# Kernel tuning notes

Hardware: AMD Instinct MI355X
Metric: run time of the kernel (lower is better)

Reference implementation:

```python
import jax, jax.numpy as jnp
import numpy as np

B = 64          # graphs per batch
N = 1500        # nodes per graph (equal sizes -> vectorized sortpool)
NT = B * N      # total nodes
DEG = 16        # avg in-degree
E_PER = N * DEG # edges per graph
F_IN = 128
K = 30          # sortpool k
LATENT = [32, 32, 32, 1]  # total 97
TOTAL_LAT = sum(LATENT)
OUT_DIM = 128


def setup_inputs() -> dict:
    key = jax.random.key(0)
    ks = jax.random.split(key, 16)
    node_feat = jax.random.normal(ks[0], (NT, F_IN), dtype=jnp.float32)
    # edges constrained within each graph (block-diagonal adjacency)
    offs = (jnp.arange(B, dtype=jnp.int32) * N)[:, None]
    edge_src = (jax.random.randint(ks[1], (B, E_PER), 0, N, dtype=jnp.int32) + offs).reshape(-1)
    edge_dst = (jax.random.randint(ks[2], (B, E_PER), 0, N, dtype=jnp.int32) + offs).reshape(-1)

    def lin(k, fan_in, shape):
        return jax.random.normal(k, shape, dtype=jnp.float32) * (1.0 / np.sqrt(fan_in))

    inp = dict(node_feat=node_feat, edge_src=edge_src, edge_dst=edge_dst)
    dims = [F_IN] + LATENT
    for i in range(4):
        inp[f'W{i+1}'] = lin(ks[3 + i], dims[i], (dims[i], dims[i + 1]))
        inp[f'b{i+1}'] = jnp.zeros((dims[i + 1],), jnp.float32)
    inp['conv1_w'] = lin(ks[8], TOTAL_LAT, (16, TOTAL_LAT))   # Conv1d(1,16,97,stride=97)
    inp['conv1_b'] = jnp.zeros((16,), jnp.float32)
    inp['conv2_w'] = lin(ks[9], 16 * 5, (32, 16, 5))          # Conv1d(16,32,5)
    inp['conv2_b'] = jnp.zeros((32,), jnp.float32)
    inp['out_w'] = lin(ks[10], 352, (352, OUT_DIM))
    inp['out_b'] = jnp.zeros((OUT_DIM,), jnp.float32)
    return inp


def reference(node_feat, edge_src, edge_dst, W1, b1, W2, b2, W3, b3, W4, b4,
              conv1_w, conv1_b, conv2_w, conv2_b, out_w, out_b):
    # node degrees (+1 for self loop), from in-edges
    deg = jax.ops.segment_sum(jnp.ones_like(edge_dst, jnp.float32), edge_dst, num_segments=NT)
    node_degs = (deg + 1.0)[:, None]

    # 4 graph-conv layers: (A @ h + h) -> Linear -> /deg -> tanh, concat features
    h = node_feat
    layers = []
    for W, b in ((W1, b1), (W2, b2), (W3, b3), (W4, b4)):
        agg = jax.ops.segment_sum(h[edge_src], edge_dst, num_segments=NT) + h
        h = jnp.tanh((agg @ W + b) / node_degs)
        layers.append(h)
    feat = jnp.concatenate(layers, axis=1)  # [NT, 97]

    # sortpooling: top-k nodes per graph by the last channel
    sort_ch = feat[:, -1].reshape(B, N)
    _, idx = jax.lax.top_k(sort_ch, K)                    # [B, K]
    gidx = (idx + (jnp.arange(B, dtype=idx.dtype) * N)[:, None]).reshape(-1)
    pooled = feat[gidx].reshape(B, K, TOTAL_LAT)          # [B, K, 97]

    # Conv1d(1,16,97,stride=97) over flattened [B,1,K*97] == per-slot linear
    c1 = jax.nn.relu(jnp.einsum('bkd,od->bok', pooled, conv1_w) + conv1_b[None, :, None])  # [B,16,K]
    mp = c1.reshape(B, 16, K // 2, 2).max(axis=-1)        # MaxPool1d(2,2) -> [B,16,15]
    c2 = jax.lax.conv_general_dilated(mp, conv2_w, (1,), 'VALID',
                                      dimension_numbers=('NCH', 'OIH', 'NCH'))
    c2 = jax.nn.relu(c2 + conv2_b[None, :, None])         # [B,32,11]
    dense = c2.reshape(B, -1)                             # [B,352]
    return jax.nn.relu(dense @ out_w + out_b)             # relu(relu(x)) == relu(x)
```

## Files before the change

kernel.cpp:

```cpp
#include <hip/hip_runtime.h>

constexpr int B = 64, N = 1500, NT = B * N;
constexpr int E_PER = 24000, E_TOT = B * E_PER;
constexpr int NQ = 4, NPQ = N / NQ;
constexpr int CAP = 9216;
constexpr int F_INN = 128, K = 30, TOT = 97;
constexpr int NB_G = 47;
constexpr int GEMM_TILES = NT / 128;

__global__ __launch_bounds__(256) void prep(const int* __restrict__ src, const int* __restrict__ dst,
                                            ushort* __restrict__ csr, int* __restrict__ rowst,
                                            int* __restrict__ degi, float* __restrict__ degf,
                                            float* __restrict__ tA,
                                            const float* __restrict__ nf, const float* __restrict__ W1) {
    __shared__ union {
        struct { int hist[NPQ]; uint4 slice[CAP / 8]; int wtot; } c;
        struct { float hs[32][128]; float Ws[32][32]; } g;
    } u;
    int bid = blockIdx.x, t = threadIdx.x;

    if (bid < B * NQ) {
        ushort* csr_l = (ushort*)u.c.slice;
        int g = bid >> 2, q = bid & 3;
        int gbase = g * N, qlo = q * NPQ;
        const int4* d4 = reinterpret_cast<const int4*>(dst + (size_t)g * E_PER);
        const int4* s4 = reinterpret_cast<const int4*>(src + (size_t)g * E_PER);

        for (int i = t; i < NPQ; i += 256) u.c.hist[i] = 0;
        __syncthreads();
        for (int i = t; i < E_PER / 4; i += 256) {
            int4 d = d4[i];
            int x0 = d.x - gbase - qlo, x1 = d.y - gbase - qlo;
            int x2 = d.z - gbase - qlo, x3 = d.w - gbase - qlo;
            if ((unsigned)x0 < (unsigned)NPQ) atomicAdd(&u.c.hist[x0], 1);
            if ((unsigned)x1 < (unsigned)NPQ) atomicAdd(&u.c.hist[x1], 1);
            if ((unsigned)x2 < (unsigned)NPQ) atomicAdd(&u.c.hist[x2], 1);
            if ((unsigned)x3 < (unsigned)NPQ) atomicAdd(&u.c.hist[x3], 1);
        }
        __syncthreads();

        int local[3];
        int sum = 0, x = 0;
        if (t < 128) {
#pragma unroll
            for (int i = 0; i < 3; ++i) {
                int v = t * 3 + i;
                int d = (v < NPQ) ? u.c.hist[v] : 0;
                local[i] = d;
                sum += (d + 7) & ~7;
            }
            x = sum;
            int lane = t & 63;
#pragma unroll
            for (int m = 1; m < 64; m <<= 1) {
                int y = __shfl_up(x, m, 64);
                if (lane >= m) x += y;
            }
        }
        if (t == 63) u.c.wtot = x;
        __syncthreads();
        if (t < 128) {
            int base = (t >= 64) ? u.c.wtot : 0;
            int run = base + x - sum;
            int rbase = (g * NQ + q) * CAP;
#pragma unroll
            for (int i = 0; i < 3; ++i) {
                int v = t * 3 + i;
                if (v < NPQ) {
                    int gv = gbase + qlo + v;
                    rowst[gv] = rbase + run;
                    degi[gv] = local[i];
                    degf[gv] = (float)(local[i] + 1);
                    u.c.hist[v] = run;
                    run += (local[i] + 7) & ~7;
                }
            }
        }
        __syncthreads();
        for (int i = t; i < E_PER / 4; i += 256) {
            int4 d = d4[i];
            int4 s = s4[i];
            int x0 = d.x - gbase - qlo, x1 = d.y - gbase - qlo;
            int x2 = d.z - gbase - qlo, x3 = d.w - gbase - qlo;
            if ((unsigned)x0 < (unsigned)NPQ) { int p = atomicAdd(&u.c.hist[x0], 1); csr_l[p] = (ushort)(s.x - gbase); }
            if ((unsigned)x1 < (unsigned)NPQ) { int p = atomicAdd(&u.c.hist[x1], 1); csr_l[p] = (ushort)(s.y - gbase); }
            if ((unsigned)x2 < (unsigned)NPQ) { int p = atomicAdd(&u.c.hist[x2], 1); csr_l[p] = (ushort)(s.z - gbase); }
            if ((unsigned)x3 < (unsigned)NPQ) { int p = atomicAdd(&u.c.hist[x3], 1); csr_l[p] = (ushort)(s.w - gbase); }
        }
        __syncthreads();
        for (int v = t; v < NPQ; v += 256)
            for (int sft = u.c.hist[v]; sft & 7; ++sft) csr_l[sft] = (ushort)(qlo + v);
        __syncthreads();
        uint4* cg = reinterpret_cast<uint4*>(csr + (size_t)(g * NQ + q) * CAP);
        for (int i = t; i < CAP / 8; i += 256)
            cg[i] = u.c.slice[i];
    } else {
        int tile = bid - B * NQ;
        int wv = t >> 6, lane = t & 63;
        int v0 = tile * 128;
        int og = wv * 8;
        float acc[2][8];
#pragma unroll
        for (int i = 0; i < 2; ++i)
#pragma unroll
            for (int j = 0; j < 8; ++j) acc[i][j] = 0.f;

        for (int kc = 0; kc < F_INN; kc += 32) {
            __syncthreads();
            {
                int n = t >> 1, kh = (t & 1) * 16;
                const float* hp = nf + (size_t)(v0 + n) * F_INN + kc + kh;
                const float4* hp4 = reinterpret_cast<const float4*>(hp);
                float4 a = hp4[0], b = hp4[1], c = hp4[2], d = hp4[3];
                u.g.hs[kh + 0][n] = a.x;  u.g.hs[kh + 1][n] = a.y;  u.g.hs[kh + 2][n] = a.z;  u.g.hs[kh + 3][n] = a.w;
                u.g.hs[kh + 4][n] = b.x;  u.g.hs[kh + 5][n] = b.y;  u.g.hs[kh + 6][n] = b.z;  u.g.hs[kh + 7][n] = b.w;
                u.g.hs[kh + 8][n] = c.x;  u.g.hs[kh + 9][n] = c.y;  u.g.hs[kh + 10][n] = c.z; u.g.hs[kh + 11][n] = c.w;
                u.g.hs[kh + 12][n] = d.x; u.g.hs[kh + 13][n] = d.y; u.g.hs[kh + 14][n] = d.z; u.g.hs[kh + 15][n] = d.w;
                int r = t >> 3, c4 = (t & 7) * 4;
                float4 w = *reinterpret_cast<const float4*>(W1 + (size_t)(kc + r) * 32 + c4);
                *reinterpret_cast<float4*>(&u.g.Ws[r][c4]) = w;
            }
            __syncthreads();
#pragma unroll
            for (int k = 0; k < 32; ++k) {
                float2 hv = *reinterpret_cast<const float2*>(&u.g.hs[k][2 * lane]);
                float4 w0 = *reinterpret_cast<const float4*>(&u.g.Ws[k][og]);
                float4 w1 = *reinterpret_cast<const float4*>(&u.g.Ws[k][og + 4]);
                acc[0][0] += hv.x * w0.x; acc[0][1] += hv.x * w0.y; acc[0][2] += hv.x * w0.z; acc[0][3] += hv.x * w0.w;
                acc[0][4] += hv.x * w1.x; acc[0][5] += hv.x * w1.y; acc[0][6] += hv.x * w1.z; acc[0][7] += hv.x * w1.w;
                acc[1][0] += hv.y * w0.x; acc[1][1] += hv.y * w0.y; acc[1][2] += hv.y * w0.z; acc[1][3] += hv.y * w0.w;
                acc[1][4] += hv.y * w1.x; acc[1][5] += hv.y * w1.y; acc[1][6] += hv.y * w1.z; acc[1][7] += hv.y * w1.w;
            }
        }
#pragma unroll
        for (int i = 0; i < 2; ++i) {
            float* op = tA + (size_t)(v0 + 2 * lane + i) * 32 + og;
            float4 r0 = {acc[i][0], acc[i][1], acc[i][2], acc[i][3]};
            float4 r1 = {acc[i][4], acc[i][5], acc[i][6], acc[i][7]};
            reinterpret_cast<float4*>(op)[0] = r0;
            reinterpret_cast<float4*>(op)[1] = r1;
        }
    }
}

template <int FUSE>
__global__ __launch_bounds__(256) void agg_f(const float* __restrict__ t,
                                             const ushort* __restrict__ csr, const int* __restrict__ rowst,
                                             const int* __restrict__ degi, const float* __restrict__ degf,
                                             const float* __restrict__ bias, const float* __restrict__ Wn,
                                             float* __restrict__ hout, float* __restrict__ tn) {
    __shared__ float Ws[1024];
    __shared__ float outs[32][32];
    if (FUSE == 32) {
        for (int i = threadIdx.x; i < 1024; i += 256) Ws[i] = Wn[i];
    }
    int bid = blockIdx.x;
    int xcd = bid & 7, j = bid >> 3;
    int g = xcd + 8 * (j / NB_G);
    int nb = j % NB_G;
    int nl = threadIdx.x >> 3;
    int f4 = threadIdx.x & 7;
    int vl = nb * 32 + nl;
    bool valid = vl < N;
    int v = g * N + vl;
    int gb8 = g * N * 8;
    const float4* t4v = reinterpret_cast<const float4*>(t);
    float4 out = {0.f, 0.f, 0.f, 0.f};
    if (valid) {
        float4 tself = t4v[(unsigned)(v * 8 + f4)];
        int e0 = rowst[v];
        int dc = degi[v];
        int pc = (dc + 7) & ~7;
        float scale = (float)(1 + dc - pc);
        float4 acc = {scale * tself.x, scale * tself.y, scale * tself.z, scale * tself.w};
        float4 s1 = {0.f, 0.f, 0.f, 0.f}, s2 = {0.f, 0.f, 0.f, 0.f};
        float4 s3 = {0.f, 0.f, 0.f, 0.f}, s4v = {0.f, 0.f, 0.f, 0.f};
        for (int e = 0; e < pc; e += 8) {
            ushort4 ia = *reinterpret_cast<const ushort4*>(csr + e0 + e);
            ushort4 ib = *reinterpret_cast<const ushort4*>(csr + e0 + e + 4);
            float4 x0 = t4v[(unsigned)(gb8 + ia.x * 8 + f4)];
            float4 x1 = t4v[(unsigned)(gb8 + ia.y * 8 + f4)];
            float4 x2 = t4v[(unsigned)(gb8 + ia.z * 8 + f4)];
            float4 x3 = t4v[(unsigned)(gb8 + ia.w * 8 + f4)];
            float4 x4 = t4v[(unsigned)(gb8 + ib.x * 8 + f4)];
            float4 x5 = t4v[(unsigned)(gb8 + ib.y * 8 + f4)];
            float4 x6 = t4v[(unsigned)(gb8 + ib.z * 8 + f4)];
            float4 x7 = t4v[(unsigned)(gb8 + ib.w * 8 + f4)];
            s1.x += x0.x + x1.x; s1.y += x0.y + x1.y; s1.z += x0.z + x1.z; s1.w += x0.w + x1.w;
            s2.x += x2.x + x3.x; s2.y += x2.y + x3.y; s2.z += x2.z + x3.z; s2.w += x2.w + x3.w;
            s3.x += x4.x + x5.x; s3.y += x4.y + x5.y; s3.z += x4.z + x5.z; s3.w += x4.w + x5.w;
            s4v.x += x6.x + x7.x; s4v.y += x6.y + x7.y; s4v.z += x6.z + x7.z; s4v.w += x6.w + x7.w;
        }
        acc.x += (s1.x + s2.x) + (s3.x + s4v.x);
        acc.y += (s1.y + s2.y) + (s3.y + s4v.y);
        acc.z += (s1.z + s2.z) + (s3.z + s4v.z);
        acc.w += (s1.w + s2.w) + (s3.w + s4v.w);
        float4 bv = *reinterpret_cast<const float4*>(bias + f4 * 4);
        float inv = 1.0f / degf[v];
        out.x = tanhf((acc.x + bv.x) * inv);
        out.y = tanhf((acc.y + bv.y) * inv);
        out.z = tanhf((acc.z + bv.z) * inv);
        out.w = tanhf((acc.w + bv.w) * inv);
        reinterpret_cast<float4*>(hout)[(unsigned)(v * 8 + f4)] = out;
    }
    if (FUSE == 32) {
        *reinterpret_cast<float4*>(&outs[nl][f4 * 4]) = out;
        __syncthreads();
        if (valid) {
            float4 s = {0.f, 0.f, 0.f, 0.f};
#pragma unroll
            for (int ff = 0; ff < 32; ++ff) {
                float h = outs[nl][ff];
                float4 wr = *reinterpret_cast<const float4*>(&Ws[ff * 32 + f4 * 4]);
                s.x += h * wr.x; s.y += h * wr.y; s.z += h * wr.z; s.w += h * wr.w;
            }
            reinterpret_cast<float4*>(tn)[(unsigned)(v * 8 + f4)] = s;
        }
    } else if (valid) {
        float4 w4 = *reinterpret_cast<const float4*>(Wn + f4 * 4);
        float p = out.x * w4.x + out.y * w4.y + out.z * w4.z + out.w * w4.w;
        p += __shfl_xor(p, 4, 64);
        p += __shfl_xor(p, 2, 64);
        p += __shfl_xor(p, 1, 64);
        if (f4 == 0) tn[v] = p;
    }
}

__global__ __launch_bounds__(512) void sort_head(const float* __restrict__ hc1, const float* __restrict__ hc2,
                                                 const float* __restrict__ hc3, const float* __restrict__ t4,
                                                 const ushort* __restrict__ csr, const int* __restrict__ rowst,
                                                 const int* __restrict__ degi, const float* __restrict__ degf,
                                                 const float* __restrict__ b4,
                                                 const float* __restrict__ c1w, const float* __restrict__ c1b,
                                                 const float* __restrict__ c2w, const float* __restrict__ c2b,
                                                 const float* __restrict__ ow, const float* __restrict__ ob,
                                                 float* __restrict__ out) {
    __shared__ float ts[N];
    __shared__ unsigned int svals[N];
    __shared__ float fvals[N];
    __shared__ int hist[2048];
    __shared__ int canA[N], canB[N];
    __shared__ int winners[32];
    __shared__ int wsum[8];
    __shared__ int st_need, st_ncand, st_tb, st_cab, st_nwin;
    __shared__ int topk_s[K];
    __shared__ float pooled[K][TOT];
    __shared__ float c1[16][K];
    __shared__ float mp[16][16];
    __shared__ float dense[352];
    __shared__ float part[4][128];

    int g = blockIdx.x, t = threadIdx.x;
    int gbase = g * N;
    int lane = t & 63, w = t >> 6;

    for (int v = t; v < N; v += 512) ts[v] = t4[gbase + v];
    if (t == 0) { st_need = K; st_nwin = 0; }
    __syncthreads();
    {
        float b4v = b4[0];
        for (int v = t; v < N; v += 512) {
            int gv = gbase + v;
            int e0 = rowst[gv], dc = degi[gv];
            int pc = (dc + 7) & ~7;
            float scale = (float)(1 + dc - pc);
            float a0 = 0.f, a1 = 0.f, a2 = 0.f, a3 = 0.f;
            for (int e = 0; e < pc; e += 4) {
                ushort4 s4 = *reinterpret_cast<const ushort4*>(csr + e0 + e);
                a0 += ts[s4.x];
                a1 += ts[s4.y];
                a2 += ts[s4.z];
                a3 += ts[s4.w];
            }
            float h = tanhf((scale * ts[v] + (a0 + a1) + (a2 + a3) + b4v) / degf[gv]);
            fvals[v] = h;
            unsigned int b = __float_as_uint(h);
            svals[v] = (b & 0x80000000u) ? ~b : (b | 0x80000000u);
        }
    }
    __syncthreads();

    auto mkkey = [&](int idx) {
        return ((unsigned long long)svals[idx] << 31) | (unsigned int)(0x7FFFFFFF - idx);
    };

    const int SHIFTS[6] = {52, 41, 30, 19, 8, 0};
    int curN = N;
    int src = 0;
    for (int pass = 0; pass < 6; ++pass) {
        int shift = SHIFTS[pass];
        int mask = (pass == 5) ? 0xFF : 0x7FF;
        for (int i = t; i < 2048; i += 512) hist[i] = 0;
        if (t == 0) st_ncand = 0;
        __syncthreads();
        for (int i = t; i < curN; i += 512) {
            int idx = (src == 0) ? i : (src == 1 ? canA[i] : canB[i]);
            int d = (int)((mkkey(idx) >> shift) & mask);
            atomicAdd(&hist[d], 1);
        }
        __syncthreads();
        int need = st_need;
        int c[4];
        int s = 0;
#pragma unroll
        for (int u = 0; u < 4; ++u) { c[u] = hist[2047 - (4 * t + u)]; s += c[u]; }
        int x = s;
#pragma unroll
        for (int m = 1; m < 64; m <<= 1) {
            int y = __shfl_up(x, m, 64);
            if (lane >= m) x += y;
        }
        if (lane == 63) wsum[w] = x;
        __syncthreads();
        int woff = 0;
        for (int ww = 0; ww < w; ++ww) woff += wsum[ww];
        int A = woff + x - s;
#pragma unroll
        for (int u = 0; u < 4; ++u) {
            if (A < need && need <= A + c[u]) { st_tb = 2047 - (4 * t + u); st_cab = A; }
            A += c[u];
        }
        __syncthreads();
        int tb = st_tb, cab = st_cab;
        int* dst = (src == 1) ? canB : canA;
        for (int i = t; i < curN; i += 512) {
            int idx = (src == 0) ? i : (src == 1 ? canA[i] : canB[i]);
            int d = (int)((mkkey(idx) >> shift) & mask);
            if (d > tb) {
                int p = atomicAdd(&st_nwin, 1);
                winners[p] = idx;
            } else if (d == tb) {
                int p = atomicAdd(&st_ncand, 1);
                dst[p] = idx;
            }
        }
        __syncthreads();
        int ncand = st_ncand;
        need -= cab;
        if (t == 0) st_need = need;
        if (ncand == need) {
            int base = st_nwin;
            for (int i = t; i < ncand; i += 512) winners[base + i] = dst[i];
            __syncthreads();
            break;
        }
        curN = ncand;
        src = (src == 1) ? 2 : 1;
        __syncthreads();
    }

    if (t < 64) {
        unsigned long long key = (t < K) ? mkkey(winners[t]) : 0ull;
        unsigned long long kk = ~key;
#pragma unroll
        for (int k = 2; k <= 64; k <<= 1) {
#pragma unroll
            for (int j = k >> 1; j > 0; j >>= 1) {
                unsigned long long o = __shfl_xor(kk, j, 64);
                bool keepMin = ((t & j) == 0) == ((t & k) == 0);
                kk = keepMin ? (kk < o ? kk : o) : (kk > o ? kk : o);
            }
        }
        key = ~kk;
        if (t < K) topk_s[t] = 0x7FFFFFFF - (int)(unsigned int)(key & 0x7FFFFFFFu);
    }
    __syncthreads();

    for (int i = t; i < K * TOT; i += 512) {
        int k = i / TOT, d = i % TOT;
        int vloc = topk_s[k];
        int gi = gbase + vloc;
        float val = (d < 32) ? hc1[(size_t)gi * 32 + d]
                  : (d < 64) ? hc2[(size_t)gi * 32 + d - 32]
                  : (d < 96) ? hc3[(size_t)gi * 32 + d - 64]
                             : fvals[vloc];
        pooled[k][d] = val;
    }
    __syncthreads();
    for (int i = t; i < 16 * K; i += 512) {
        int o = i / K, k = i % K;
        float s = c1b[o];
        for (int d = 0; d < TOT; ++d) s += pooled[k][d] * c1w[o * TOT + d];
        c1[o][k] = fmaxf(s, 0.f);
    }
    __syncthreads();
    for (int i = t; i < 16 * 15; i += 512) {
        int o = i / 15, p = i % 15;
        mp[o][p] = fmaxf(c1[o][2 * p], c1[o][2 * p + 1]);
    }
    __syncthreads();
    for (int i = t; i < 352; i += 512) {
        int o = i / 11, p = i % 11;
        float s = c2b[o];
#pragma unroll
        for (int ci = 0; ci < 16; ++ci)
#pragma unroll
            for (int tt = 0; tt < 5; ++tt)
                s += mp[ci][p + tt] * c2w[(o * 16 + ci) * 5 + tt];
        dense[i] = fmaxf(s, 0.f);
    }
    __syncthreads();
    {
        int o = t & 127, q = t >> 7;
        float s = 0.f;
        for (int m = q * 88; m < (q + 1) * 88; ++m) s += dense[m] * ow[m * 128 + o];
        part[q][o] = s;
    }
    __syncthreads();
    if (t < 128) {
        float s = (part[0][t] + part[1][t]) + (part[2][t] + part[3][t]) + ob[t];
        out[g * 128 + t] = fmaxf(s, 0.f);
    }
}

extern "C" void kernel_launch(void* const* d_in, const int* in_sizes, int n_in,
                              void* d_out, int out_size, void* d_ws, size_t ws_size,
                              hipStream_t stream) {
    const float* node_feat = (const float*)d_in[0];
    const int* esrc = (const int*)d_in[1];
    const int* edst = (const int*)d_in[2];
    const float* W1 = (const float*)d_in[3];
    const float* b1 = (const float*)d_in[4];
    const float* W2 = (const float*)d_in[5];
    const float* b2 = (const float*)d_in[6];
    const float* W3 = (const float*)d_in[7];
    const float* b3 = (const float*)d_in[8];
    const float* W4 = (const float*)d_in[9];
    const float* b4 = (const float*)d_in[10];
    const float* c1w = (const float*)d_in[11];
    const float* c1b = (const float*)d_in[12];
    const float* c2w = (const float*)d_in[13];
    const float* c2b = (const float*)d_in[14];
    const float* ow = (const float*)d_in[15];
    const float* ob = (const float*)d_in[16];

    char* ws = (char*)d_ws;
    size_t off = 0;
    auto alloc = [&](size_t bytes) {
        size_t r = off;
        off += (bytes + 255) & ~(size_t)255;
        return r;
    };
    int* deg_i = (int*)(ws + alloc((size_t)NT * 4));
    int* rowst = (int*)(ws + alloc((size_t)NT * 4));
    float* degf = (float*)(ws + alloc((size_t)NT * 4));
    ushort* csr = (ushort*)(ws + alloc((size_t)B * NQ * CAP * 2));
    float* tA = (float*)(ws + alloc((size_t)NT * 32 * 4));
    float* tB = (float*)(ws + alloc((size_t)NT * 32 * 4));
    float* hc1 = (float*)(ws + alloc((size_t)NT * 32 * 4));
    float* hc2 = (float*)(ws + alloc((size_t)NT * 32 * 4));
    float* hc3 = (float*)(ws + alloc((size_t)NT * 32 * 4));
    float* t4 = (float*)(ws + alloc((size_t)NT * 4));

    prep<<<B * NQ + GEMM_TILES, 256, 0, stream>>>(esrc, edst, csr, rowst, deg_i, degf,
                                                  tA, node_feat, W1);

    agg_f<32><<<8 * NB_G * 8, 256, 0, stream>>>(tA, csr, rowst, deg_i, degf, b1, W2, hc1, tB);
    agg_f<32><<<8 * NB_G * 8, 256, 0, stream>>>(tB, csr, rowst, deg_i, degf, b2, W3, hc2, tA);
    agg_f<1><<<8 * NB_G * 8, 256, 0, stream>>>(tA, csr, rowst, deg_i, degf, b3, W4, hc3, t4);

    sort_head<<<B, 512, 0, stream>>>(hc1, hc2, hc3, t4, csr, rowst, deg_i, degf, b4,
                                     c1w, c1b, c2w, c2b, ow, ob, (float*)d_out);
}
```

Baseline: 116.7 us.

## Sort nodes by degree per quarter-graph to balance aggregation wavefront work

The prep kernel now counting-sorts each quarter-graph's nodes by in-degree and writes a permutation array. The aggregation kernels read node indices through this permutation, with 12 blocks per quarter and NB_G raised to 48, so nodes of similar degree share a wavefront. The aim is to cut divergence from the variable-length edge loops. In exchange it adds an indirect load per node and scatters the output writes, which are no longer contiguous.

```diff
diff --git a/kernel.cpp b/kernel.cpp
--- a/kernel.cpp
+++ b/kernel.cpp
@@ -4,17 +4,19 @@
 constexpr int E_PER = 24000, E_TOT = B * E_PER;
 constexpr int NQ = 4, NPQ = N / NQ;
 constexpr int CAP = 9216;
+constexpr int PERM_STRIDE = 384;
 constexpr int F_INN = 128, K = 30, TOT = 97;
-constexpr int NB_G = 47;
+constexpr int NB_G = 48;
 constexpr int GEMM_TILES = NT / 128;
 
 __global__ __launch_bounds__(256) void prep(const int* __restrict__ src, const int* __restrict__ dst,
                                             ushort* __restrict__ csr, int* __restrict__ rowst,
                                             int* __restrict__ degi, float* __restrict__ degf,
+                                            ushort* __restrict__ perm,
                                             float* __restrict__ tA,
                                             const float* __restrict__ nf, const float* __restrict__ W1) {
     __shared__ union {
-        struct { int hist[NPQ]; uint4 slice[CAP / 8]; int wtot; } c;
+        struct { int hist[NPQ]; uint4 slice[CAP / 8]; int wtot; int dh[64]; } c;
         struct { float hs[32][128]; float Ws[32][32]; } g;
     } u;
     int bid = blockIdx.x, t = threadIdx.x;
@@ -27,6 +29,7 @@
         const int4* s4 = reinterpret_cast<const int4*>(src + (size_t)g * E_PER);
 
         for (int i = t; i < NPQ; i += 256) u.c.hist[i] = 0;
+        if (t < 64) u.c.dh[t] = 0;
         __syncthreads();
         for (int i = t; i < E_PER / 4; i += 256) {
             int4 d = d4[i];
@@ -48,6 +51,7 @@
                 int d = (v < NPQ) ? u.c.hist[v] : 0;
                 local[i] = d;
                 sum += (d + 7) & ~7;
+                if (v < NPQ) atomicAdd(&u.c.dh[min(d, 63)], 1);
             }
             x = sum;
             int lane = t & 63;
@@ -59,6 +63,9 @@
         }
         if (t == 63) u.c.wtot = x;
         __syncthreads();
+        int myDeg[3];
+#pragma unroll
+        for (int i = 0; i < 3; ++i) myDeg[i] = (t < 128) ? local[i] : 0;
         if (t < 128) {
             int base = (t >= 64) ? u.c.wtot : 0;
             int run = base + x - sum;
@@ -77,6 +84,28 @@
             }
         }
         __syncthreads();
+        if (t < 64) {
+            int c = u.c.dh[t];
+            int xx = c;
+#pragma unroll
+            for (int m = 1; m < 64; m <<= 1) {
+                int y = __shfl_up(xx, m, 64);
+                if (t >= m) xx += y;
+            }
+            u.c.dh[t] = xx - c;
+        }
+        __syncthreads();
+        if (t < 128) {
+            ushort* pg = perm + (size_t)(g * NQ + q) * PERM_STRIDE;
+#pragma unroll
+            for (int i = 0; i < 3; ++i) {
+                int v = t * 3 + i;
+                if (v < NPQ) {
+                    int pos = atomicAdd(&u.c.dh[min(myDeg[i], 63)], 1);
+                    pg[pos] = (ushort)v;
+                }
+            }
+        }
         for (int i = t; i < E_PER / 4; i += 256) {
             int4 d = d4[i];
             int4 s = s4[i];
@@ -147,6 +176,7 @@
 __global__ __launch_bounds__(256) void agg_f(const float* __restrict__ t,
                                              const ushort* __restrict__ csr, const int* __restrict__ rowst,
                                              const int* __restrict__ degi, const float* __restrict__ degf,
+                                             const ushort* __restrict__ perm,
                                              const float* __restrict__ bias, const float* __restrict__ Wn,
                                              float* __restrict__ hout, float* __restrict__ tn) {
     __shared__ float Ws[1024];
@@ -158,10 +188,13 @@
     int xcd = bid & 7, j = bid >> 3;
     int g = xcd + 8 * (j / NB_G);
     int nb = j % NB_G;
+    int q = nb / 12, slot = nb % 12;
     int nl = threadIdx.x >> 3;
     int f4 = threadIdx.x & 7;
-    int vl = nb * 32 + nl;
-    bool valid = vl < N;
+    int idx = slot * 32 + nl;
+    bool valid = idx < NPQ;
+    int vl = 0;
+    if (valid) vl = q * NPQ + perm[(size_t)(g * NQ + q) * PERM_STRIDE + idx];
     int v = g * N + vl;
     int gb8 = g * N * 8;
     const float4* t4v = reinterpret_cast<const float4*>(t);
@@ -445,6 +478,7 @@
     int* rowst = (int*)(ws + alloc((size_t)NT * 4));
     float* degf = (float*)(ws + alloc((size_t)NT * 4));
     ushort* csr = (ushort*)(ws + alloc((size_t)B * NQ * CAP * 2));
+    ushort* perm = (ushort*)(ws + alloc((size_t)B * NQ * PERM_STRIDE * 2));
     float* tA = (float*)(ws + alloc((size_t)NT * 32 * 4));
     float* tB = (float*)(ws + alloc((size_t)NT * 32 * 4));
     float* hc1 = (float*)(ws + alloc((size_t)NT * 32 * 4));
@@ -453,11 +487,11 @@
     float* t4 = (float*)(ws + alloc((size_t)NT * 4));
 
     prep<<<B * NQ + GEMM_TILES, 256, 0, stream>>>(esrc, edst, csr, rowst, deg_i, degf,
-                                                  tA, node_feat, W1);
-
-    agg_f<32><<<8 * NB_G * 8, 256, 0, stream>>>(tA, csr, rowst, deg_i, degf, b1, W2, hc1, tB);
-    agg_f<32><<<8 * NB_G * 8, 256, 0, stream>>>(tB, csr, rowst, deg_i, degf, b2, W3, hc2, tA);
-    agg_f<1><<<8 * NB_G * 8, 256, 0, stream>>>(tA, csr, rowst, deg_i, degf, b3, W4, hc3, t4);
+                                                  perm, tA, node_feat, W1);
+
+    agg_f<32><<<8 * NB_G * 8, 256, 0, stream>>>(tA, csr, rowst, deg_i, degf, perm, b1, W2, hc1, tB);
+    agg_f<32><<<8 * NB_G * 8, 256, 0, stream>>>(tB, csr, rowst, deg_i, degf, perm, b2, W3, hc2, tA);
+    agg_f<1><<<8 * NB_G * 8, 256, 0, stream>>>(tA, csr, rowst, deg_i, degf, perm, b3, W4, hc3, t4);
 
     sort_head<<<B, 512, 0, stream>>>(hc1, hc2, hc3, t4, csr, rowst, deg_i, degf, b4,
                                      c1w, c1b, c2w, c2b, ow, ob, (float*)d_out);
```

New measurement: 113.3 us. -2.9%, faster.
